# Optimization experiments

Measured on AMD Instinct MI355X. Metric: run time of the kernel, lower is better.

Reference implementation:

```python
import jax, jax.numpy as jnp
import numpy as np

B, T, D = 4, 256, 512          # batch, seq_len, encoder_dim
L, H = 2, 8                    # num xLSTM blocks, num heads
I = 2 * D                      # inner dim (proj_factor=2)
DH = I // H                    # per-head dim = 128
K, G = 32, 64                  # mdn_components, goal_dim
EPS = 1e-5


def _ln(x, s, b):
    m = x.mean(-1, keepdims=True)
    v = jnp.mean((x - m) ** 2, -1, keepdims=True)
    return (x - m) * jax.lax.rsqrt(v + EPS) * s + b


def setup_inputs() -> dict:
    key = jax.random.key(0)
    ks = jax.random.split(key, 16)
    sc = 0.02
    nrm = lambda k, shp: jax.random.normal(k, shp, jnp.float32) * sc
    return {
        "x": jax.random.normal(ks[0], (B, T, D), jnp.float32),
        "ln_s": jnp.ones((L, D), jnp.float32),
        "ln_b": jnp.zeros((L, D), jnp.float32),
        "W_proj": nrm(ks[1], (L, D, 2 * I)),
        "Wq": nrm(ks[2], (L, I, I)),
        "Wk": nrm(ks[3], (L, I, I)),
        "Wv": nrm(ks[4], (L, I, I)),
        "Wi": nrm(ks[5], (L, I, H)),
        "bi": jnp.zeros((L, H), jnp.float32),
        "Wf": nrm(ks[6], (L, I, H)),
        "bf": jnp.full((L, H), 3.0, jnp.float32),  # forget-gate bias init
        "gn_s": jnp.ones((L, I), jnp.float32),
        "gn_b": jnp.zeros((L, I), jnp.float32),
        "W_down": nrm(ks[7], (L, I, D)),
        "fln_s": jnp.ones((D,), jnp.float32),
        "fln_b": jnp.zeros((D,), jnp.float32),
        "W_pi": nrm(ks[8], (D, K)),
        "b_pi": jnp.zeros((K,), jnp.float32),
        "W_mu": nrm(ks[9], (D, K * G)),
        "b_mu": jnp.zeros((K * G,), jnp.float32),
        "W_sig": nrm(ks[10], (D, K * G)),
        "b_sig": jnp.zeros((K * G,), jnp.float32),
    }


def _forward(x, ln_s, ln_b, W_proj, Wq, Wk, Wv, Wi, bi, Wf, bf,
             gn_s, gn_b, W_down, fln_s, fln_b,
             W_pi, b_pi, W_mu, b_mu, W_sig, b_sig):
    inv_sqrt_dh = 1.0 / (DH ** 0.5)

    def step(carry, x_t):  # x_t: (B, D); replicates per-timestep xlstm_stack.step()
        C, n, m = carry    # (L,B,H,DH,DH), (L,B,H,DH), (L,B,H)
        h = x_t
        for l in range(L):  # fixed small block loop
            skip = h
            xn = _ln(h, ln_s[l], ln_b[l])
            xp = xn @ W_proj[l]                      # (B, 2I)
            xm, z = jnp.split(xp, 2, axis=-1)        # mLSTM branch / gate branch
            q = (xm @ Wq[l]).reshape(B, H, DH)
            k = (xm @ Wk[l]).reshape(B, H, DH) * inv_sqrt_dh
            v = (xm @ Wv[l]).reshape(B, H, DH)
            ip = xm @ Wi[l] + bi[l]                  # (B, H) exp input gate preact
            fp = xm @ Wf[l] + bf[l]                  # (B, H) forget gate preact
            logf = jax.nn.log_sigmoid(fp)
            m_new = jnp.maximum(logf + m[l], ip)     # stabilizer
            ig = jnp.exp(ip - m_new)
            fg = jnp.exp(logf + m[l] - m_new)
            # matrix memory update: C <- f*C + i * k v^T ; n <- f*n + i*k
            C_new = fg[:, :, None, None] * C[l] + ig[:, :, None, None] * (k[..., :, None] * v[..., None, :])
            n_new = fg[..., None] * n[l] + ig[..., None] * k
            num = jnp.einsum('bhk,bhkv->bhv', q, C_new)
            den = jnp.maximum(jnp.abs(jnp.einsum('bhk,bhk->bh', q, n_new)), 1.0)
            hh = num / den[..., None]                # (B, H, DH)
            # multi-head norm (per-head layernorm, no per-head affine)
            mu_h = hh.mean(-1, keepdims=True)
            var_h = jnp.mean((hh - mu_h) ** 2, -1, keepdims=True)
            hh = (hh - mu_h) * jax.lax.rsqrt(var_h + EPS)
            hh = hh.reshape(B, I) * gn_s[l] + gn_b[l]
            hh = hh * jax.nn.silu(z)                 # output gating branch
            h = skip + hh @ W_down[l]                # residual
            C = C.at[l].set(C_new)
            n = n.at[l].set(n_new)
            m = m.at[l].set(m_new)
        return (C, n, m), h

    C0 = jnp.zeros((L, B, H, DH, DH), x.dtype)
    n0 = jnp.zeros((L, B, H, DH), x.dtype)
    m0 = jnp.zeros((L, B, H), x.dtype)
    _, hs = jax.lax.scan(step, (C0, n0, m0), jnp.swapaxes(x, 0, 1))
    last = _ln(hs[-1], fln_s, fln_b)                 # post-blocks norm on final step
    pi = jax.nn.softmax(last @ W_pi + b_pi, axis=-1)              # (B, K)
    mu = (last @ W_mu + b_mu).reshape(B, K, G)                     # (B, K, G)
    sigma = jax.nn.softplus(last @ W_sig + b_sig).reshape(B, K, G) # (B, K, G)
    return pi, mu, sigma


def reference(x, ln_s, ln_b, W_proj, Wq, Wk, Wv, Wi, bi, Wf, bf,
              gn_s, gn_b, W_down, fln_s, fln_b,
              W_pi, b_pi, W_mu, b_mu, W_sig, b_sig):
    return _forward(x, ln_s, ln_b, W_proj, Wq, Wk, Wv, Wi, bi, Wf, bf,
                    gn_s, gn_b, W_down, fln_s, fln_b,
                    W_pi, b_pi, W_mu, b_mu, W_sig, b_sig)
```

## Files before the change

### kernel.cpp

```cpp
#include <hip/hip_runtime.h>
#include <hip/hip_bf16.h>
#include <math.h>

#define DEV __device__ __forceinline__

typedef __attribute__((ext_vector_type(8))) short bf16x8;
typedef __attribute__((ext_vector_type(4))) float f32x4;

static DEV float softplus_f(float x){ return fmaxf(x,0.f) + log1pf(expf(-fabsf(x))); }
static DEV float logsig_f(float x){ return fminf(x,0.f) - log1pf(expf(-fabsf(x))); }
static DEV float silu_f(float x){ return x / (1.f + expf(-x)); }
static DEV unsigned short f2bf(float f){
  union { float f; unsigned u; } v; v.f = f;
  unsigned r = (v.u + 0x7fffu + ((v.u >> 16) & 1u)) >> 16;
  return (unsigned short)r;
}
static DEV float bf2f(unsigned short u){
  union { unsigned u; float f; } v; v.u = ((unsigned)u) << 16; return v.f;
}
static DEV void load_lds16(const unsigned short* g, unsigned short* lds){
  __builtin_amdgcn_global_load_lds(
      (const __attribute__((address_space(1))) void*)g,
      (__attribute__((address_space(3))) void*)lds, 16, 0, 0);
}

__global__ __launch_bounds__(256) void wprep(
    const float* __restrict__ Wp, const float* __restrict__ Wq,
    const float* __restrict__ Wk, const float* __restrict__ Wv,
    const float* __restrict__ Wd, const float* __restrict__ Wi,
    const float* __restrict__ Wf,
    unsigned short* projT0, unsigned short* projT1,
    unsigned short* qT0, unsigned short* kT0, unsigned short* kT1,
    unsigned short* vT0, unsigned short* vT1, unsigned short* dT0,
    float* __restrict__ Wc)
{
  int bid = blockIdx.x;
  if (bid >= 1920){
    int fb = bid - 1920;
    int gid = fb * 4 + (threadIdx.x >> 6);
    int l = gid >> 9, d = gid & 511;
    int lane = threadIdx.x & 63;
    const float* wp = Wp + (size_t)l*512*2048 + (size_t)d*2048 + lane*16;
    const float* wi = Wi + (size_t)l*1024*8;
    const float* wf = Wf + (size_t)l*1024*8;
    float acc[16];
    #pragma unroll
    for (int q = 0; q < 16; ++q) acc[q] = 0.f;
    #pragma unroll 4
    for (int u = 0; u < 16; ++u){
      float xv = wp[u];
      int j = lane*16 + u;
      float4 wi0 = *(const float4*)(wi + j*8);
      float4 wi1 = *(const float4*)(wi + j*8 + 4);
      float4 wf0 = *(const float4*)(wf + j*8);
      float4 wf1 = *(const float4*)(wf + j*8 + 4);
      acc[0]  = fmaf(xv, wi0.x, acc[0]);  acc[1]  = fmaf(xv, wi0.y, acc[1]);
      acc[2]  = fmaf(xv, wi0.z, acc[2]);  acc[3]  = fmaf(xv, wi0.w, acc[3]);
      acc[4]  = fmaf(xv, wi1.x, acc[4]);  acc[5]  = fmaf(xv, wi1.y, acc[5]);
      acc[6]  = fmaf(xv, wi1.z, acc[6]);  acc[7]  = fmaf(xv, wi1.w, acc[7]);
      acc[8]  = fmaf(xv, wf0.x, acc[8]);  acc[9]  = fmaf(xv, wf0.y, acc[9]);
      acc[10] = fmaf(xv, wf0.z, acc[10]); acc[11] = fmaf(xv, wf0.w, acc[11]);
      acc[12] = fmaf(xv, wf1.x, acc[12]); acc[13] = fmaf(xv, wf1.y, acc[13]);
      acc[14] = fmaf(xv, wf1.z, acc[14]); acc[15] = fmaf(xv, wf1.w, acc[15]);
    }
    #pragma unroll
    for (int o = 32; o > 0; o >>= 1){
      #pragma unroll
      for (int q = 0; q < 16; ++q) acc[q] += __shfl_xor(acc[q], o);
    }
    if (lane == 0){
      float* dst = Wc + (size_t)l*512*16 + d*16;
      #pragma unroll
      for (int q = 0; q < 16; ++q) dst[q] = acc[q];
    }
    return;
  }
  int z, t;
  if (bid < 512){ z = bid >> 8; t = bid & 255; }
  else if (bid < 1792){ z = 2 + ((bid - 512) >> 8); t = (bid - 512) & 255; }
  else { z = 7; t = bid - 1792; }
  const float* W; unsigned short* Wt; int K, M; float scale = 1.f;
  const float INV = 0.08838834764831845f;
  switch (z){
    case 0: W = Wp;              Wt = projT0; K = 512;  M = 2048; break;
    case 1: W = Wp + 512*2048;   Wt = projT1; K = 512;  M = 2048; break;
    case 2: W = Wq;              Wt = qT0;    K = 1024; M = 1024; break;
    case 3: W = Wk;              Wt = kT0;    K = 1024; M = 1024; scale = INV; break;
    case 4: W = Wk + 1048576;    Wt = kT1;    K = 1024; M = 1024; scale = INV; break;
    case 5: W = Wv;              Wt = vT0;    K = 1024; M = 1024; break;
    case 6: W = Wv + 1048576;    Wt = vT1;    K = 1024; M = 1024; break;
    default: W = Wd;             Wt = dT0;    K = 1024; M = 512;  break;
  }
  int mtiles = M >> 6;
  int mt = t % mtiles, kt = t / mtiles;
  int m0 = mt * 64, k0 = kt * 64;
  __shared__ float s[64][65];
  int tx = threadIdx.x & 15, ty = threadIdx.x >> 4;
  #pragma unroll
  for (int u = 0; u < 64; u += 16){
    int r = u + ty;
    *(float4*)&s[r][tx*4] = *(const float4*)(W + (size_t)(k0+r)*M + m0 + tx*4);
  }
  __syncthreads();
  #pragma unroll
  for (int u = 0; u < 64; u += 16){
    int mr = u + ty;
    ushort4 o;
    o.x = f2bf(s[tx*4+0][mr] * scale);
    o.y = f2bf(s[tx*4+1][mr] * scale);
    o.z = f2bf(s[tx*4+2][mr] * scale);
    o.w = f2bf(s[tx*4+3][mr] * scale);
    *(ushort4*)(Wt + (size_t)(m0+mr)*K + k0 + tx*4) = o;
  }
}

__global__ __launch_bounds__(256) void ln_gates(
    const float* __restrict__ in, unsigned short* __restrict__ outb,
    const float* __restrict__ s, const float* __restrict__ b,
    const float* __restrict__ Wc, float* __restrict__ ipfp)
{
  int r = blockIdx.x;
  const float* x = in + (size_t)r * 512;
  int tid = threadIdx.x;
  float lsum = 0.f, lsq = 0.f;
  for (int i = tid; i < 512; i += 256){ float v = x[i]; lsum += v; lsq += v*v; }
  #pragma unroll
  for (int o = 32; o > 0; o >>= 1){ lsum += __shfl_down(lsum, o); lsq += __shfl_down(lsq, o); }
  __shared__ float s1[4], s2[4];
  int wid = tid >> 6, lane = tid & 63;
  if (lane == 0){ s1[wid] = lsum; s2[wid] = lsq; }
  __syncthreads();
  if (tid == 0){ float a=0.f,c=0.f; for (int w=0; w<4; ++w){ a+=s1[w]; c+=s2[w]; } s1[0]=a; s2[0]=c; }
  __syncthreads();
  float mean = s1[0] * (1.f/512.f);
  float var  = s2[0] * (1.f/512.f) - mean*mean;
  float rstd = rsqrtf(var + 1e-5f);
  __shared__ float P[256][17];
  float g[16];
  #pragma unroll
  for (int q = 0; q < 16; ++q) g[q] = 0.f;
  for (int i = tid; i < 512; i += 256){
    float v = (x[i]-mean)*rstd*s[i] + b[i];
    outb[(size_t)r*512 + i] = f2bf(v);
    const float* wrow = Wc + i*16;
    #pragma unroll
    for (int q = 0; q < 16; ++q) g[q] = fmaf(v, wrow[q], g[q]);
  }
  #pragma unroll
  for (int q = 0; q < 16; ++q) P[tid][q] = g[q];
  __syncthreads();
  {
    int q = tid >> 4, c = tid & 15;
    float sacc = 0.f;
    #pragma unroll
    for (int u = 0; u < 16; ++u) sacc += P[c*16 + u][q];
    sacc += __shfl_xor(sacc, 1); sacc += __shfl_xor(sacc, 2);
    sacc += __shfl_xor(sacc, 4); sacc += __shfl_xor(sacc, 8);
    if (c == 0) ipfp[r*16 + q] = sacc;
  }
}

__global__ __launch_bounds__(256) void gemm_mfma128_multi(
    const unsigned short* __restrict__ A, int lda,
    const unsigned short* __restrict__ Bt0, const unsigned short* __restrict__ Bt1,
    const unsigned short* __restrict__ Bt2, int ldb,
    unsigned short* __restrict__ C0, unsigned short* __restrict__ C1,
    unsigned short* __restrict__ C2, int ldc, int K)
{
  const unsigned short* Bt = (blockIdx.z == 0) ? Bt0 : (blockIdx.z == 1) ? Bt1 : Bt2;
  unsigned short* Cbf      = (blockIdx.z == 0) ? C0  : (blockIdx.z == 1) ? C1  : C2;
  __shared__ __align__(16) unsigned short As[8192];
  __shared__ __align__(16) unsigned short Bs[8192];
  int row0 = blockIdx.y * 128, col0 = blockIdx.x * 128;
  int tid = threadIdx.x;
  int w = tid >> 6, l = tid & 63;
  int wr = (w >> 1) * 64, wc = (w & 1) * 64;
  int lrm = l & 15, lk = l >> 4;
  int lr3 = l >> 3;
  int scc = (l & 7) ^ lr3;
  f32x4 acc[4][4] = {};
  for (int k0 = 0; k0 < K; k0 += 64){
    #pragma unroll
    for (int it = 0; it < 4; ++it){
      int rowA = (it*4 + w)*8 + lr3;
      load_lds16(A  + (size_t)(row0 + rowA)*lda + k0 + scc*8, &As[(it*4 + w)*512]);
      load_lds16(Bt + (size_t)(col0 + rowA)*ldb + k0 + scc*8, &Bs[(it*4 + w)*512]);
    }
    __syncthreads();
    #pragma unroll
    for (int kk = 0; kk < 2; ++kk){
      int q = kk*4 + lk;
      bf16x8 af[4], bfr[4];
      #pragma unroll
      for (int i = 0; i < 4; ++i){
        int ra = wr + i*16 + lrm;
        af[i] = *(const bf16x8*)&As[ra*64 + ((q ^ (ra & 7)) << 3)];
      }
      #pragma unroll
      for (int j = 0; j < 4; ++j){
        int rb = wc + j*16 + lrm;
        bfr[j] = *(const bf16x8*)&Bs[rb*64 + ((q ^ (rb & 7)) << 3)];
      }
      #pragma unroll
      for (int i = 0; i < 4; ++i)
        #pragma unroll
        for (int j = 0; j < 4; ++j)
          acc[i][j] = __builtin_amdgcn_mfma_f32_16x16x32_bf16(af[i], bfr[j], acc[i][j], 0, 0, 0);
    }
    __syncthreads();
  }
  #pragma unroll
  for (int i = 0; i < 4; ++i){
    #pragma unroll
    for (int j = 0; j < 4; ++j){
      int col = col0 + wc + j*16 + lrm;
      #pragma unroll
      for (int r = 0; r < 4; ++r){
        int row = row0 + wr + i*16 + lk*4 + r;
        Cbf[(size_t)row*ldc + col] = f2bf(acc[i][j][r]);
      }
    }
  }
}

__global__ __launch_bounds__(256) void gemm_mfma(
    const unsigned short* __restrict__ A, int lda,
    const unsigned short* __restrict__ Bt, int ldb,
    float* __restrict__ C, int ldc,
    unsigned short* __restrict__ Cbf,
    const float* __restrict__ skip, int ldskip,
    int K)
{
  __shared__ __align__(16) unsigned short As[64][72];
  __shared__ __align__(16) unsigned short Bs[64][72];
  int row0 = blockIdx.y * 64, col0 = blockIdx.x * 64;
  int tid = threadIdx.x;
  int w = tid >> 6, l = tid & 63;
  int wr = (w >> 1) * 32, wc = (w & 1) * 32;
  int lr = l & 15, lk = l >> 4;
  int r1 = tid >> 3, c1 = (tid & 7) * 8;
  int r2 = (tid + 256) >> 3, c2 = ((tid + 256) & 7) * 8;
  const unsigned short* a1 = A  + (size_t)(row0 + r1) * lda + c1;
  const unsigned short* a2 = A  + (size_t)(row0 + r2) * lda + c2;
  const unsigned short* b1 = Bt + (size_t)(col0 + r1) * ldb + c1;
  const unsigned short* b2 = Bt + (size_t)(col0 + r2) * ldb + c2;
  f32x4 acc00 = {0,0,0,0}, acc01 = {0,0,0,0}, acc10 = {0,0,0,0}, acc11 = {0,0,0,0};
  for (int k0 = 0; k0 < K; k0 += 64){
    *(bf16x8*)&As[r1][c1] = *(const bf16x8*)(a1 + k0);
    *(bf16x8*)&As[r2][c2] = *(const bf16x8*)(a2 + k0);
    *(bf16x8*)&Bs[r1][c1] = *(const bf16x8*)(b1 + k0);
    *(bf16x8*)&Bs[r2][c2] = *(const bf16x8*)(b2 + k0);
    __syncthreads();
    #pragma unroll
    for (int kk = 0; kk < 2; ++kk){
      bf16x8 a0 = *(const bf16x8*)&As[wr + lr][kk*32 + lk*8];
      bf16x8 a1f = *(const bf16x8*)&As[wr + 16 + lr][kk*32 + lk*8];
      bf16x8 b0 = *(const bf16x8*)&Bs[wc + lr][kk*32 + lk*8];
      bf16x8 b1f = *(const bf16x8*)&Bs[wc + 16 + lr][kk*32 + lk*8];
      acc00 = __builtin_amdgcn_mfma_f32_16x16x32_bf16(a0, b0, acc00, 0, 0, 0);
      acc01 = __builtin_amdgcn_mfma_f32_16x16x32_bf16(a0, b1f, acc01, 0, 0, 0);
      acc10 = __builtin_amdgcn_mfma_f32_16x16x32_bf16(a1f, b0, acc10, 0, 0, 0);
      acc11 = __builtin_amdgcn_mfma_f32_16x16x32_bf16(a1f, b1f, acc11, 0, 0, 0);
    }
    __syncthreads();
  }
  #pragma unroll
  for (int i = 0; i < 2; ++i){
    #pragma unroll
    for (int j = 0; j < 2; ++j){
      f32x4 a = (i == 0) ? ((j == 0) ? acc00 : acc01) : ((j == 0) ? acc10 : acc11);
      int col = col0 + wc + j*16 + lr;
      #pragma unroll
      for (int r = 0; r < 4; ++r){
        int row = row0 + wr + i*16 + lk*4 + r;
        float o = a[r];
        if (skip) o += skip[(size_t)row*ldskip + col];
        if (C)   C[(size_t)row*ldc + col] = o;
        if (Cbf) Cbf[(size_t)row*ldc + col] = f2bf(o);
      }
    }
  }
}

__global__ __launch_bounds__(256) void attn_l0_mfma(
    const unsigned short* __restrict__ q, const unsigned short* __restrict__ k,
    const unsigned short* __restrict__ v,
    const float* __restrict__ ipfp, const float* __restrict__ bi, const float* __restrict__ bfg,
    const unsigned short* __restrict__ xpb,
    const float* __restrict__ gn_s, const float* __restrict__ gn_b,
    unsigned short* __restrict__ gated)
{
  __shared__ __align__(16) char smem[48128];
  unsigned short (*Ks)[136] = (unsigned short(*)[136])smem;
  unsigned short (*Vt)[72]  = (unsigned short(*)[72])(smem + 17408);
  unsigned short (*Ps)[72]  = (unsigned short(*)[72])(smem + 35840);
  float* invden = (float*)(smem + 45056);
  float (*denL)[64] = (float(*)[64])(smem + 45568);
  float* alpha_full = (float*)(smem + 46080);
  float* Mt_full    = (float*)(smem + 47104);
  float (*numf)[140] = (float(*)[140])smem;

  int blk = blockIdx.x;
  int tt = blk & 3, h = (blk >> 2) & 7, b = blk >> 5;
  int t0 = tt * 64;
  int tid = threadIdx.x;
  int w = tid >> 6, l = tid & 63;
  int wr = (w >> 1) * 32;
  int wc = (w & 1) * 32;
  int wd = (w & 1) * 64;
  int lrm = l & 15, lk = l >> 4;
  size_t headoff = (size_t)h * 128;

  {
    #pragma unroll
    for (int u = 0; u < 4; ++u){
      int o = u*256 + tid, row = o >> 4, oct = o & 15;
      *(bf16x8*)&Ks[row][oct*8] =
        *(const bf16x8*)(q + (size_t)(b*256 + t0 + row)*1024 + headoff + oct*8);
    }
    if (tid < 64){
      int lane = tid;
      float bih = bi[h], bfh = bfg[h];
      float lf[4], ip4[4];
      #pragma unroll
      for (int u = 0; u < 4; ++u){
        int r = b*256 + lane*4 + u;
        ip4[u] = ipfp[r*16 + h] + bih;
        lf[u]  = logsig_f(ipfp[r*16 + 8 + h] + bfh);
      }
      float c0 = lf[0], c1 = c0+lf[1], c2 = c1+lf[2], c3 = c2+lf[3];
      float tot = c3, pre = tot;
      #pragma unroll
      for (int o = 1; o < 64; o <<= 1){ float vv = __shfl_up(pre, o); if (lane >= o) pre += vv; }
      float excl = pre - tot;
      float al[4] = { ip4[0]-(excl+c0), ip4[1]-(excl+c1), ip4[2]-(excl+c2), ip4[3]-(excl+c3) };
      float lm[4];
      lm[0]=al[0]; lm[1]=fmaxf(lm[0],al[1]); lm[2]=fmaxf(lm[1],al[2]); lm[3]=fmaxf(lm[2],al[3]);
      float pm = lm[3];
      #pragma unroll
      for (int o = 1; o < 64; o <<= 1){ float vv = __shfl_up(pm, o); if (lane >= o) pm = fmaxf(pm, vv); }
      float pmexcl = __shfl_up(pm, 1);
      if (lane == 0) pmexcl = -3.4e38f;
      #pragma unroll
      for (int u = 0; u < 4; ++u){
        alpha_full[lane*4+u] = al[u];
        Mt_full[lane*4+u] = fmaxf(0.f, fmaxf(pmexcl, lm[u]));
      }
    }
    if (tid < 128) ((float*)denL)[tid] = 0.f;
  }
  __syncthreads();
  bf16x8 aq[2][4];
  #pragma unroll
  for (int i = 0; i < 2; ++i)
    #pragma unroll
    for (int kk = 0; kk < 4; ++kk)
      aq[i][kk] = *(const bf16x8*)&Ks[wr + i*16 + lrm][kk*32 + lk*8];
  __syncthreads();

  f32x4 pacc[2][4] = {};
  int ntile = tt + 1;

  for (int it = 0; it < ntile; ++it){
    int s0 = it * 64;
    #pragma unroll
    for (int u = 0; u < 4; ++u){
      int o = u*256 + tid, row = o >> 4, oct = o & 15;
      *(bf16x8*)&Ks[row][oct*8] =
        *(const bf16x8*)(k + (size_t)(b*256 + s0 + row)*1024 + headoff + oct*8);
    }
    #pragma unroll
    for (int u = 0; u < 2; ++u){
      int task = u*256 + tid;
      int sp = task & 31, oct = task >> 5;
      const unsigned short* vp = v + (size_t)(b*256 + s0 + sp*2)*1024 + headoff + oct*8;
      bf16x8 r0 = *(const bf16x8*)vp;
      bf16x8 r1 = *(const bf16x8*)(vp + 1024);
      #pragma unroll
      for (int j = 0; j < 8; ++j){
        unsigned lo = (unsigned short)r0[j];
        unsigned hi = (unsigned short)r1[j];
        *(unsigned*)&Vt[oct*8 + j][sp*2] = lo | (hi << 16);
      }
    }
    __syncthreads();

    f32x4 sacc[2][2] = {};
    #pragma unroll
    for (int kk = 0; kk < 4; ++kk){
      bf16x8 b0 = *(const bf16x8*)&Ks[wc + lrm][kk*32 + lk*8];
      bf16x8 b1 = *(const bf16x8*)&Ks[wc + 16 + lrm][kk*32 + lk*8];
      sacc[0][0] = __builtin_amdgcn_mfma_f32_16x16x32_bf16(aq[0][kk], b0, sacc[0][0], 0, 0, 0);
      sacc[0][1] = __builtin_amdgcn_mfma_f32_16x16x32_bf16(aq[0][kk], b1, sacc[0][1], 0, 0, 0);
      sacc[1][0] = __builtin_amdgcn_mfma_f32_16x16x32_bf16(aq[1][kk], b0, sacc[1][0], 0, 0, 0);
      sacc[1][1] = __builtin_amdgcn_mfma_f32_16x16x32_bf16(aq[1][kk], b1, sacc[1][1], 0, 0, 0);
    }

    bool diag = (it == ntile - 1);
    float av0 = alpha_full[s0 + wc + lrm];
    float av1 = alpha_full[s0 + wc + 16 + lrm];
    #pragma unroll
    for (int i = 0; i < 2; ++i){
      #pragma unroll
      for (int r = 0; r < 4; ++r){
        int tl = wr + i*16 + lk*4 + r;
        float mt = Mt_full[t0 + tl];
        float p0 = __expf(av0 - mt) * sacc[i][0][r];
        float p1 = __expf(av1 - mt) * sacc[i][1][r];
        if (diag){
          if (wc + lrm      > tl) p0 = 0.f;
          if (wc + 16 + lrm > tl) p1 = 0.f;
        }
        Ps[tl][wc + lrm]      = f2bf(p0);
        Ps[tl][wc + 16 + lrm] = f2bf(p1);
        float dv = p0 + p1;
        dv += __shfl_xor(dv, 1); dv += __shfl_xor(dv, 2);
        dv += __shfl_xor(dv, 4); dv += __shfl_xor(dv, 8);
        if (lrm == 0) denL[w & 1][tl] += dv;
      }
    }
    __syncthreads();

    #pragma unroll
    for (int ks = 0; ks < 2; ++ks){
      bf16x8 pa0 = *(const bf16x8*)&Ps[wr + lrm][ks*32 + lk*8];
      bf16x8 pa1 = *(const bf16x8*)&Ps[wr + 16 + lrm][ks*32 + lk*8];
      #pragma unroll
      for (int jd = 0; jd < 4; ++jd){
        bf16x8 vb8 = *(const bf16x8*)&Vt[wd + jd*16 + lrm][ks*32 + lk*8];
        pacc[0][jd] = __builtin_amdgcn_mfma_f32_16x16x32_bf16(pa0, vb8, pacc[0][jd], 0, 0, 0);
        pacc[1][jd] = __builtin_amdgcn_mfma_f32_16x16x32_bf16(pa1, vb8, pacc[1][jd], 0, 0, 0);
      }
    }
    __syncthreads();
  }

  #pragma unroll
  for (int i = 0; i < 2; ++i)
    #pragma unroll
    for (int jd = 0; jd < 4; ++jd)
      #pragma unroll
      for (int r = 0; r < 4; ++r)
        numf[wr + i*16 + lk*4 + r][wd + jd*16 + lrm] = pacc[i][jd][r];
  if (tid < 64){
    float s = denL[0][tid] + denL[1][tid];
    invden[tid] = 1.0f / fmaxf(fabsf(s), 1.0f);
  }
  __syncthreads();

  {
    int row = tid >> 2, qq = tid & 3;
    float inv = invden[row];
    const float* nr = &numf[row][qq*32];
    float xs[32];
    float sum = 0.f, sq = 0.f;
    #pragma unroll
    for (int j = 0; j < 8; ++j){
      float4 t4 = *(const float4*)(nr + j*4);
      float v0 = t4.x*inv, v1 = t4.y*inv, v2 = t4.z*inv, v3 = t4.w*inv;
      xs[j*4+0] = v0; xs[j*4+1] = v1; xs[j*4+2] = v2; xs[j*4+3] = v3;
      sum += v0+v1+v2+v3;
      sq  += v0*v0+v1*v1+v2*v2+v3*v3;
    }
    sum += __shfl_xor(sum, 1); sq += __shfl_xor(sq, 1);
    sum += __shfl_xor(sum, 2); sq += __shfl_xor(sq, 2);
    float mean = sum * (1.f/128.f);
    float var  = sq  * (1.f/128.f) - mean*mean;
    float rstd = rsqrtf(var + 1e-5f);
    int rr = b*256 + t0 + row;
    const unsigned short* zp = xpb + (size_t)rr*2048 + 1024 + headoff + qq*32;
    const float* gsP = gn_s + headoff + qq*32;
    const float* gbP = gn_b + headoff + qq*32;
    unsigned short* op = gated + (size_t)rr*1024 + headoff + qq*32;
    #pragma unroll
    for (int j8 = 0; j8 < 4; ++j8){
      bf16x8 zv = *(const bf16x8*)(zp + j8*8);
      bf16x8 ov;
      #pragma unroll
      for (int j = 0; j < 8; ++j){
        int jj = j8*8 + j;
        float valn = (xs[jj]-mean)*rstd*gsP[jj] + gbP[jj];
        ov[j] = (short)f2bf(valn * silu_f(bf2f((unsigned short)zv[j])));
      }
      *(bf16x8*)(op + j8*8) = ov;
    }
  }
}

__global__ void qlast_split(const unsigned short* __restrict__ xpb, const float* __restrict__ Wq1,
                            float* __restrict__ part)
{
  int jt = blockIdx.x, ks = blockIdx.y;
  int j = jt*256 + threadIdx.x;
  __shared__ float xs[4][32];
  int t = threadIdx.x;
  if (t < 128){ int b = t >> 5, kk = t & 31; xs[b][kk] = bf2f(xpb[(size_t)(b*256+255)*2048 + ks*32 + kk]); }
  __syncthreads();
  float a0=0.f,a1=0.f,a2=0.f,a3=0.f;
  #pragma unroll 8
  for (int kk = 0; kk < 32; ++kk){
    float wv = Wq1[(size_t)(ks*32+kk)*1024 + j];
    a0 = fmaf(xs[0][kk], wv, a0);
    a1 = fmaf(xs[1][kk], wv, a1);
    a2 = fmaf(xs[2][kk], wv, a2);
    a3 = fmaf(xs[3][kk], wv, a3);
  }
  part[((size_t)ks*4 + 0)*1024 + j] = a0;
  part[((size_t)ks*4 + 1)*1024 + j] = a1;
  part[((size_t)ks*4 + 2)*1024 + j] = a2;
  part[((size_t)ks*4 + 3)*1024 + j] = a3;
}

__global__ __launch_bounds__(256) void attn_l1_split(
    const float* __restrict__ qpart, const unsigned short* __restrict__ k1,
    const unsigned short* __restrict__ v1,
    const float* __restrict__ ipfp, const float* __restrict__ bi, const float* __restrict__ bfg,
    float* __restrict__ pnum, float* __restrict__ pden)
{
  int sc = blockIdx.x, bh = blockIdx.y;
  int b = bh >> 3, h = bh & 7;
  int s0 = sc * 32;
  int tid = threadIdx.x;
  __shared__ float qsh[128];
  __shared__ float alpha256[256];
  __shared__ float mt255s;
  __shared__ float sred[32][9];
  __shared__ float as[32];
  __shared__ float nred[2][128];
  if (tid < 128){
    float s = 0.f;
    #pragma unroll 8
    for (int ks = 0; ks < 32; ++ks) s += qpart[((size_t)ks*4 + b)*1024 + h*128 + tid];
    qsh[tid] = s;
  }
  if (tid >= 128 && tid < 192){
    int lane = tid - 128;
    float bih = bi[h], bfh = bfg[h];
    float lf[4], ip4[4];
    #pragma unroll
    for (int u = 0; u < 4; ++u){
      int r = b*256 + lane*4 + u;
      ip4[u] = ipfp[r*16 + h] + bih;
      lf[u]  = logsig_f(ipfp[r*16 + 8 + h] + bfh);
    }
    float c0 = lf[0], c1 = c0+lf[1], c2 = c1+lf[2], c3 = c2+lf[3];
    float tot = c3, pre = tot;
    #pragma unroll
    for (int o = 1; o < 64; o <<= 1){ float vv = __shfl_up(pre, o); if (lane >= o) pre += vv; }
    float excl = pre - tot;
    float al[4] = { ip4[0]-(excl+c0), ip4[1]-(excl+c1), ip4[2]-(excl+c2), ip4[3]-(excl+c3) };
    #pragma unroll
    for (int u = 0; u < 4; ++u) alpha256[lane*4+u] = al[u];
    float mx = fmaxf(fmaxf(al[0],al[1]), fmaxf(al[2],al[3]));
    #pragma unroll
    for (int o = 32; o > 0; o >>= 1) mx = fmaxf(mx, __shfl_xor(mx, o));
    if (lane == 0) mt255s = fmaxf(0.f, mx);
  }
  __syncthreads();
  {
    int sl = tid & 31, dc = tid >> 5;
    const unsigned short* kp = k1 + (size_t)(b*256 + s0 + sl)*1024 + h*128 + dc*16;
    float p = 0.f;
    #pragma unroll
    for (int u = 0; u < 16; u += 8){
      bf16x8 kv = *(const bf16x8*)(kp + u);
      #pragma unroll
      for (int e = 0; e < 8; ++e) p = fmaf(qsh[dc*16+u+e], bf2f((unsigned short)kv[e]), p);
    }
    sred[sl][dc] = p;
  }
  __syncthreads();
  if (tid < 32){
    float sum = 0.f;
    #pragma unroll
    for (int dc = 0; dc < 8; ++dc) sum += sred[tid][dc];
    float w = __expf(alpha256[s0 + tid] - mt255s);
    as[tid] = w * sum;
  }
  __syncthreads();
  {
    int d = tid & 127, sg = tid >> 7;
    const unsigned short* vp = v1 + (size_t)(b*256 + s0 + sg*16)*1024 + h*128 + d;
    float np = 0.f;
    #pragma unroll
    for (int u = 0; u < 16; ++u) np = fmaf(as[sg*16 + u], bf2f(vp[(size_t)u*1024]), np);
    nred[sg][d] = np;
  }
  __syncthreads();
  if (tid < 128) pnum[((size_t)bh*8 + sc)*128 + tid] = nred[0][tid] + nred[1][tid];
  if (tid == 128){
    float dsum = 0.f;
    #pragma unroll
    for (int u = 0; u < 32; ++u) dsum += as[u];
    pden[bh*8 + sc] = dsum;
  }
}

__global__ __launch_bounds__(128) void attn_l1_fin(
    const float* __restrict__ pnum, const float* __restrict__ pden,
    const unsigned short* __restrict__ xpb,
    const float* __restrict__ gn_s, const float* __restrict__ gn_b,
    float* __restrict__ gated1)
{
  int bh = blockIdx.x; int b = bh >> 3, h = bh & 7;
  int tid = threadIdx.x;
  __shared__ float hh[128];
  __shared__ float dsh, msh, rsh;
  float nsum = 0.f;
  #pragma unroll
  for (int sc = 0; sc < 8; ++sc) nsum += pnum[((size_t)bh*8 + sc)*128 + tid];
  if (tid == 0){
    float d = 0.f;
    #pragma unroll
    for (int sc = 0; sc < 8; ++sc) d += pden[bh*8 + sc];
    dsh = fmaxf(fabsf(d), 1.0f);
  }
  __syncthreads();
  float hv = nsum / dsh;
  hh[tid] = hv;
  __syncthreads();
  if (tid < 64){
    float a = hh[tid], c = hh[tid + 64];
    float s1 = a + c, s2v = a*a + c*c;
    #pragma unroll
    for (int o = 32; o > 0; o >>= 1){ s1 += __shfl_down(s1, o); s2v += __shfl_down(s2v, o); }
    if (tid == 0){
      float mean = s1*(1.f/128.f);
      float var  = s2v*(1.f/128.f) - mean*mean;
      msh = mean; rsh = rsqrtf(var + 1e-5f);
    }
  }
  __syncthreads();
  {
    int i = h*128 + tid;
    float valn = (hv - msh)*rsh*gn_s[i] + gn_b[i];
    float z = bf2f(xpb[(size_t)(b*256 + 255)*2048 + 1024 + i]);
    gated1[b*1024 + i] = valn * silu_f(z);
  }
}

__global__ void dl_split(const float* __restrict__ gated1, const float* __restrict__ Wd,
                         float* __restrict__ part)
{
  int jt = blockIdx.x, ks = blockIdx.y;
  int j = jt*256 + threadIdx.x;
  __shared__ float xs[4][32];
  int t = threadIdx.x;
  if (t < 128){ int b = t >> 5, kk = t & 31; xs[b][kk] = gated1[b*1024 + ks*32 + kk]; }
  __syncthreads();
  float a0=0.f,a1=0.f,a2=0.f,a3=0.f;
  #pragma unroll 8
  for (int kk = 0; kk < 32; ++kk){
    float wv = Wd[(size_t)(ks*32+kk)*512 + j];
    a0 = fmaf(xs[0][kk], wv, a0);
    a1 = fmaf(xs[1][kk], wv, a1);
    a2 = fmaf(xs[2][kk], wv, a2);
    a3 = fmaf(xs[3][kk], wv, a3);
  }
  part[((size_t)ks*4 + 0)*512 + j] = a0;
  part[((size_t)ks*4 + 1)*512 + j] = a1;
  part[((size_t)ks*4 + 2)*512 + j] = a2;
  part[((size_t)ks*4 + 3)*512 + j] = a3;
}

__global__ __launch_bounds__(256) void dl_fin(
    const float* __restrict__ part, const float* __restrict__ h0,
    const float* __restrict__ fln_s, const float* __restrict__ fln_b,
    const float* __restrict__ W_pi, const float* __restrict__ b_pi,
    float* __restrict__ lastb, float* __restrict__ out)
{
  int b = blockIdx.x;
  int tid = threadIdx.x;
  __shared__ float ls[512];
  __shared__ float pred[8][33];
  __shared__ float s1[4], s2[4];
  float v[2];
  #pragma unroll
  for (int u = 0; u < 2; ++u){
    int jj = tid*2 + u;
    float s = 0.f;
    #pragma unroll 8
    for (int ks = 0; ks < 32; ++ks) s += part[((size_t)ks*4 + b)*512 + jj];
    v[u] = h0[(size_t)(b*256 + 255)*512 + jj] + s;
  }
  float lsum = v[0] + v[1], lsq = v[0]*v[0] + v[1]*v[1];
  #pragma unroll
  for (int o = 32; o > 0; o >>= 1){ lsum += __shfl_down(lsum, o); lsq += __shfl_down(lsq, o); }
  int wid = tid >> 6, lane = tid & 63;
  if (lane == 0){ s1[wid] = lsum; s2[wid] = lsq; }
  __syncthreads();
  if (tid == 0){ float a=0.f,c=0.f; for (int w2=0; w2<4; ++w2){ a+=s1[w2]; c+=s2[w2]; } s1[0]=a; s2[0]=c; }
  __syncthreads();
  float mean = s1[0] * (1.f/512.f);
  float var  = s2[0] * (1.f/512.f) - mean*mean;
  float rstd = rsqrtf(var + 1e-5f);
  #pragma unroll
  for (int u = 0; u < 2; ++u){
    int jj = tid*2 + u;
    float lv = (v[u]-mean)*rstd*fln_s[jj] + fln_b[jj];
    lastb[b*512 + jj] = lv;
    ls[jj] = lv;
  }
  __syncthreads();
  {
    int o = tid & 31, pt = tid >> 5;
    float pa = 0.f;
    #pragma unroll 8
    for (int u = 0; u < 64; ++u){ int i = pt*64 + u; pa = fmaf(ls[i], W_pi[i*32 + o], pa); }
    pred[pt][o] = pa;
  }
  __syncthreads();
  if (tid < 32){
    float acc = b_pi[tid];
    #pragma unroll
    for (int pt = 0; pt < 8; ++pt) acc += pred[pt][tid];
    float m = acc;
    #pragma unroll
    for (int o2 = 16; o2 > 0; o2 >>= 1) m = fmaxf(m, __shfl_xor(m, o2));
    float e = __expf(acc - m);
    float ss = e;
    #pragma unroll
    for (int o2 = 16; o2 > 0; o2 >>= 1) ss += __shfl_xor(ss, o2);
    out[b*32 + tid] = e / ss;
  }
}

__global__ void ms_split(const float* __restrict__ last,
                         const float* __restrict__ W_mu, const float* __restrict__ W_sig,
                         float* __restrict__ part)
{
  int jt = blockIdx.x, ks = blockIdx.y, mat = blockIdx.z;
  int j = jt*256 + threadIdx.x;
  const float* W = mat ? W_sig : W_mu;
  __shared__ float xs[4][64];
  int t = threadIdx.x;
  { int b = t >> 6, kk = t & 63; xs[b][kk] = last[b*512 + ks*64 + kk]; }
  __syncthreads();
  float a0=0.f,a1=0.f,a2=0.f,a3=0.f;
  #pragma unroll 8
  for (int kk = 0; kk < 64; ++kk){
    float wv = W[(size_t)(ks*64+kk)*2048 + j];
    a0 = fmaf(xs[0][kk], wv, a0);
    a1 = fmaf(xs[1][kk], wv, a1);
    a2 = fmaf(xs[2][kk], wv, a2);
    a3 = fmaf(xs[3][kk], wv, a3);
  }
  size_t base = ((size_t)(mat*8 + ks)*4);
  part[(base + 0)*2048 + j] = a0;
  part[(base + 1)*2048 + j] = a1;
  part[(base + 2)*2048 + j] = a2;
  part[(base + 3)*2048 + j] = a3;
}

__global__ void ms_reduce(const float* __restrict__ part,
                          const float* __restrict__ b_mu, const float* __restrict__ b_sig,
                          float* __restrict__ out)
{
  int j = blockIdx.x*256 + threadIdx.x;
  int b = blockIdx.y, mat = blockIdx.z;
  float s = mat ? b_sig[j] : b_mu[j];
  for (int ks = 0; ks < 8; ++ks) s += part[((size_t)(mat*8 + ks)*4 + b)*2048 + j];
  out[128 + mat*8192 + b*2048 + j] = mat ? softplus_f(s) : s;
}

extern "C" void kernel_launch(void* const* d_in, const int* in_sizes, int n_in,
                              void* d_out, int out_size, void* d_ws, size_t ws_size,
                              hipStream_t stream)
{
  const float* x      = (const float*)d_in[0];
  const float* ln_s   = (const float*)d_in[1];
  const float* ln_b   = (const float*)d_in[2];
  const float* W_proj = (const float*)d_in[3];
  const float* Wq     = (const float*)d_in[4];
  const float* Wk     = (const float*)d_in[5];
  const float* Wv     = (const float*)d_in[6];
  const float* Wi     = (const float*)d_in[7];
  const float* bi     = (const float*)d_in[8];
  const float* Wf     = (const float*)d_in[9];
  const float* bf     = (const float*)d_in[10];
  const float* gn_s   = (const float*)d_in[11];
  const float* gn_b   = (const float*)d_in[12];
  const float* W_down = (const float*)d_in[13];
  const float* fln_s  = (const float*)d_in[14];
  const float* fln_b  = (const float*)d_in[15];
  const float* W_pi   = (const float*)d_in[16];
  const float* b_pi   = (const float*)d_in[17];
  const float* W_mu   = (const float*)d_in[18];
  const float* b_mu   = (const float*)d_in[19];
  const float* W_sig  = (const float*)d_in[20];
  const float* b_sig  = (const float*)d_in[21];
  float* out = (float*)d_out;

  char* p = (char*)d_ws;
  unsigned short* projT0 = (unsigned short*)p; p += (size_t)2048*512*2;
  unsigned short* projT1 = (unsigned short*)p; p += (size_t)2048*512*2;
  unsigned short* qT0    = (unsigned short*)p; p += (size_t)1024*1024*2;
  unsigned short* kT0    = (unsigned short*)p; p += (size_t)1024*1024*2;
  unsigned short* kT1    = (unsigned short*)p; p += (size_t)1024*1024*2;
  unsigned short* vT0    = (unsigned short*)p; p += (size_t)1024*1024*2;
  unsigned short* vT1    = (unsigned short*)p; p += (size_t)1024*1024*2;
  unsigned short* dT0    = (unsigned short*)p; p += (size_t)512*1024*2;
  float* Wc              = (float*)p;          p += (size_t)2*512*16*4;
  unsigned short* xnb    = (unsigned short*)p; p += (size_t)1024*512*2;
  unsigned short* xpb    = (unsigned short*)p; p += (size_t)1024*2048*2;
  unsigned short* qbb    = (unsigned short*)p; p += (size_t)1024*1024*2;
  unsigned short* kbb    = (unsigned short*)p; p += (size_t)1024*1024*2;
  unsigned short* vbb    = (unsigned short*)p; p += (size_t)1024*1024*2;
  unsigned short* gatedb = (unsigned short*)p; p += (size_t)1024*1024*2;
  float* h0     = (float*)p; p += (size_t)1024*512*4;
  float* ipfp   = (float*)p; p += (size_t)16384*4;
  float* gated1 = (float*)p; p += (size_t)4096*4;
  float* lastb  = (float*)p; p += (size_t)2048*4;
  float* qpart  = (float*)p; p += (size_t)32*4096*4;
  float* dpart  = (float*)p; p += (size_t)32*4*512*4;
  float* pnum   = (float*)p; p += (size_t)32*8*128*4;
  float* pden   = (float*)p; p += (size_t)32*8*4;
  float* mspart = (float*)p; p += (size_t)16*4*2048*4;

  const float* ln_s1 = ln_s + 512;
  const float* ln_b1 = ln_b + 512;
  const float* gn_s1 = gn_s + 1024;
  const float* gn_b1 = gn_b + 1024;
  const float* Wq1   = Wq + 1024*1024;
  const float* Wd1   = W_down + 1024*512;

  dim3 blk256(256);

  wprep<<<2176, blk256, 0, stream>>>(W_proj, Wq, Wk, Wv, W_down, Wi, Wf,
      projT0, projT1, qT0, kT0, kT1, vT0, vT1, dT0, Wc);

  ln_gates<<<1024, blk256, 0, stream>>>(x, xnb, ln_s, ln_b, Wc, ipfp);
  gemm_mfma128_multi<<<dim3(16,8,1), blk256, 0, stream>>>(xnb, 512, projT0, projT0, projT0, 512, xpb, xpb, xpb, 2048, 512);
  gemm_mfma128_multi<<<dim3(8,8,3), blk256, 0, stream>>>(xpb, 2048, qT0, kT0, vT0, 1024, qbb, kbb, vbb, 1024, 1024);
  attn_l0_mfma<<<128, blk256, 0, stream>>>(qbb, kbb, vbb, ipfp, bi, bf, xpb, gn_s, gn_b, gatedb);
  gemm_mfma<<<dim3(8,16), blk256, 0, stream>>>(gatedb, 1024, dT0, 1024, h0, 512, nullptr, x, 512, 1024);

  ln_gates<<<1024, blk256, 0, stream>>>(h0, xnb, ln_s1, ln_b1, Wc + 512*16, ipfp);
  gemm_mfma128_multi<<<dim3(16,8,1), blk256, 0, stream>>>(xnb, 512, projT1, projT1, projT1, 512, xpb, xpb, xpb, 2048, 512);
  gemm_mfma128_multi<<<dim3(8,8,2), blk256, 0, stream>>>(xpb, 2048, kT1, vT1, vT1, 1024, kbb, vbb, vbb, 1024, 1024);
  qlast_split<<<dim3(4,32), blk256, 0, stream>>>(xpb, Wq1, qpart);
  attn_l1_split<<<dim3(8,32), blk256, 0, stream>>>(qpart, kbb, vbb, ipfp, bi + 8, bf + 8, pnum, pden);
  attn_l1_fin<<<32, 128, 0, stream>>>(pnum, pden, xpb, gn_s1, gn_b1, gated1);
  dl_split<<<dim3(2,32), blk256, 0, stream>>>(gated1, Wd1, dpart);
  dl_fin<<<4, blk256, 0, stream>>>(dpart, h0, fln_s, fln_b, W_pi, b_pi, lastb, out);

  ms_split<<<dim3(8,8,2), blk256, 0, stream>>>(lastb, W_mu, W_sig, mspart);
  ms_reduce<<<dim3(8,4,2), blk256, 0, stream>>>(mspart, b_mu, b_sig, out);
}
```

Before: 192.1 us.

## Fuse split-reduce kernel pairs with last-block atomic finalization; widen weight-transpose tiles

Merges three split/finalize kernel pairs (attention layer-1, down-projection plus final norm and pi softmax, mu/sigma heads) into single kernels. The last block to finish, found through an atomic counter after a threadfence, performs the reduction, which removes three kernel launches and their serialization gaps. Counters are zeroed in the weight-prep kernel. The weight-transpose blocks now cover 128-row K tiles with 8-wide bf16 stores, halving the block count. The costs are that each finalize step runs on one block, and that correctness depends on the counter reset and memory fences.

```diff
diff --git a/kernel.cpp b/kernel.cpp
--- a/kernel.cpp
+++ b/kernel.cpp
@@ -32,11 +32,12 @@
     unsigned short* projT0, unsigned short* projT1,
     unsigned short* qT0, unsigned short* kT0, unsigned short* kT1,
     unsigned short* vT0, unsigned short* vT1, unsigned short* dT0,
-    float* __restrict__ Wc)
+    float* __restrict__ Wc, unsigned* __restrict__ cnts)
 {
   int bid = blockIdx.x;
-  if (bid >= 1920){
-    int fb = bid - 1920;
+  if (bid == 0 && threadIdx.x < 40) cnts[threadIdx.x] = 0;
+  if (bid >= 960){
+    int fb = bid - 960;
     int gid = fb * 4 + (threadIdx.x >> 6);
     int l = gid >> 9, d = gid & 511;
     int lane = threadIdx.x & 63;
@@ -76,9 +77,8 @@
     return;
   }
   int z, t;
-  if (bid < 512){ z = bid >> 8; t = bid & 255; }
-  else if (bid < 1792){ z = 2 + ((bid - 512) >> 8); t = (bid - 512) & 255; }
-  else { z = 7; t = bid - 1792; }
+  if (bid < 896){ z = bid >> 7; t = bid & 127; }
+  else { z = 7; t = bid - 896; }
   const float* W; unsigned short* Wt; int K, M; float scale = 1.f;
   const float INV = 0.08838834764831845f;
   switch (z){
@@ -93,11 +93,11 @@
   }
   int mtiles = M >> 6;
   int mt = t % mtiles, kt = t / mtiles;
-  int m0 = mt * 64, k0 = kt * 64;
-  __shared__ float s[64][65];
+  int m0 = mt * 64, k0 = kt * 128;
+  __shared__ float s[128][65];
   int tx = threadIdx.x & 15, ty = threadIdx.x >> 4;
   #pragma unroll
-  for (int u = 0; u < 64; u += 16){
+  for (int u = 0; u < 128; u += 16){
     int r = u + ty;
     *(float4*)&s[r][tx*4] = *(const float4*)(W + (size_t)(k0+r)*M + m0 + tx*4);
   }
@@ -105,12 +105,10 @@
   #pragma unroll
   for (int u = 0; u < 64; u += 16){
     int mr = u + ty;
-    ushort4 o;
-    o.x = f2bf(s[tx*4+0][mr] * scale);
-    o.y = f2bf(s[tx*4+1][mr] * scale);
-    o.z = f2bf(s[tx*4+2][mr] * scale);
-    o.w = f2bf(s[tx*4+3][mr] * scale);
-    *(ushort4*)(Wt + (size_t)(m0+mr)*K + k0 + tx*4) = o;
+    bf16x8 o;
+    #pragma unroll
+    for (int e = 0; e < 8; ++e) o[e] = (short)f2bf(s[tx*8+e][mr] * scale);
+    *(bf16x8*)(Wt + (size_t)(m0+mr)*K + k0 + tx*8) = o;
   }
 }
 
@@ -515,7 +513,10 @@
     const float* __restrict__ qpart, const unsigned short* __restrict__ k1,
     const unsigned short* __restrict__ v1,
     const float* __restrict__ ipfp, const float* __restrict__ bi, const float* __restrict__ bfg,
-    float* __restrict__ pnum, float* __restrict__ pden)
+    const unsigned short* __restrict__ xpb,
+    const float* __restrict__ gn_s, const float* __restrict__ gn_b,
+    float* __restrict__ pnum, float* __restrict__ pden,
+    float* __restrict__ gated1, unsigned* __restrict__ cnts)
 {
   int sc = blockIdx.x, bh = blockIdx.y;
   int b = bh >> 3, h = bh & 7;
@@ -594,59 +595,60 @@
     for (int u = 0; u < 32; ++u) dsum += as[u];
     pden[bh*8 + sc] = dsum;
   }
-}
-
-__global__ __launch_bounds__(128) void attn_l1_fin(
-    const float* __restrict__ pnum, const float* __restrict__ pden,
-    const unsigned short* __restrict__ xpb,
-    const float* __restrict__ gn_s, const float* __restrict__ gn_b,
-    float* __restrict__ gated1)
-{
-  int bh = blockIdx.x; int b = bh >> 3, h = bh & 7;
-  int tid = threadIdx.x;
-  __shared__ float hh[128];
-  __shared__ float dsh, msh, rsh;
-  float nsum = 0.f;
-  #pragma unroll
-  for (int sc = 0; sc < 8; ++sc) nsum += pnum[((size_t)bh*8 + sc)*128 + tid];
+  __threadfence();
+  __shared__ int lastF;
+  if (tid == 0) lastF = (atomicAdd(&cnts[2 + bh], 1u) == 7u) ? 1 : 0;
+  __syncthreads();
+  if (!lastF) return;
+  __shared__ float hh2[128];
+  __shared__ float dsh2, msh2, rsh2;
   if (tid == 0){
     float d = 0.f;
     #pragma unroll
-    for (int sc = 0; sc < 8; ++sc) d += pden[bh*8 + sc];
-    dsh = fmaxf(fabsf(d), 1.0f);
-  }
-  __syncthreads();
-  float hv = nsum / dsh;
-  hh[tid] = hv;
+    for (int s2 = 0; s2 < 8; ++s2) d += pden[bh*8 + s2];
+    dsh2 = fmaxf(fabsf(d), 1.0f);
+  }
+  __syncthreads();
+  if (tid < 128){
+    float nsum = 0.f;
+    #pragma unroll
+    for (int s2 = 0; s2 < 8; ++s2) nsum += pnum[((size_t)bh*8 + s2)*128 + tid];
+    hh2[tid] = nsum / dsh2;
+  }
   __syncthreads();
   if (tid < 64){
-    float a = hh[tid], c = hh[tid + 64];
+    float a = hh2[tid], c = hh2[tid + 64];
     float s1 = a + c, s2v = a*a + c*c;
     #pragma unroll
     for (int o = 32; o > 0; o >>= 1){ s1 += __shfl_down(s1, o); s2v += __shfl_down(s2v, o); }
     if (tid == 0){
       float mean = s1*(1.f/128.f);
       float var  = s2v*(1.f/128.f) - mean*mean;
-      msh = mean; rsh = rsqrtf(var + 1e-5f);
-    }
-  }
-  __syncthreads();
-  {
+      msh2 = mean; rsh2 = rsqrtf(var + 1e-5f);
+    }
+  }
+  __syncthreads();
+  if (tid < 128){
     int i = h*128 + tid;
-    float valn = (hv - msh)*rsh*gn_s[i] + gn_b[i];
+    float valn = (hh2[tid] - msh2)*rsh2*gn_s[i] + gn_b[i];
     float z = bf2f(xpb[(size_t)(b*256 + 255)*2048 + 1024 + i]);
     gated1[b*1024 + i] = valn * silu_f(z);
   }
 }
 
-__global__ void dl_split(const float* __restrict__ gated1, const float* __restrict__ Wd,
-                         float* __restrict__ part)
+__global__ __launch_bounds__(256) void dl_all(
+    const float* __restrict__ gated1, const float* __restrict__ Wd,
+    const float* __restrict__ h0,
+    const float* __restrict__ fln_s, const float* __restrict__ fln_b,
+    const float* __restrict__ W_pi, const float* __restrict__ b_pi,
+    float* __restrict__ part, float* __restrict__ lastb, float* __restrict__ out,
+    unsigned* __restrict__ cnts)
 {
   int jt = blockIdx.x, ks = blockIdx.y;
   int j = jt*256 + threadIdx.x;
+  int tid = threadIdx.x;
   __shared__ float xs[4][32];
-  int t = threadIdx.x;
-  if (t < 128){ int b = t >> 5, kk = t & 31; xs[b][kk] = gated1[b*1024 + ks*32 + kk]; }
+  if (tid < 128){ int b = tid >> 5, kk = tid & 31; xs[b][kk] = gated1[b*1024 + ks*32 + kk]; }
   __syncthreads();
   float a0=0.f,a1=0.f,a2=0.f,a3=0.f;
   #pragma unroll 8
@@ -661,80 +663,81 @@
   part[((size_t)ks*4 + 1)*512 + j] = a1;
   part[((size_t)ks*4 + 2)*512 + j] = a2;
   part[((size_t)ks*4 + 3)*512 + j] = a3;
-}
-
-__global__ __launch_bounds__(256) void dl_fin(
-    const float* __restrict__ part, const float* __restrict__ h0,
-    const float* __restrict__ fln_s, const float* __restrict__ fln_b,
-    const float* __restrict__ W_pi, const float* __restrict__ b_pi,
-    float* __restrict__ lastb, float* __restrict__ out)
-{
-  int b = blockIdx.x;
+  __threadfence();
+  __shared__ int lastF;
+  if (tid == 0) lastF = (atomicAdd(&cnts[0], 1u) == 63u) ? 1 : 0;
+  __syncthreads();
+  if (!lastF) return;
+  __shared__ float ls2[512];
+  __shared__ float pred2[8][33];
+  __shared__ float s1[4], s2[4];
+  for (int b2 = 0; b2 < 4; ++b2){
+    float v[2];
+    #pragma unroll
+    for (int u = 0; u < 2; ++u){
+      int jj = tid*2 + u;
+      float s = 0.f;
+      #pragma unroll 8
+      for (int k2 = 0; k2 < 32; ++k2) s += part[((size_t)k2*4 + b2)*512 + jj];
+      v[u] = h0[(size_t)(b2*256 + 255)*512 + jj] + s;
+    }
+    float lsum = v[0] + v[1], lsq = v[0]*v[0] + v[1]*v[1];
+    #pragma unroll
+    for (int o = 32; o > 0; o >>= 1){ lsum += __shfl_down(lsum, o); lsq += __shfl_down(lsq, o); }
+    int wid = tid >> 6, lane = tid & 63;
+    if (lane == 0){ s1[wid] = lsum; s2[wid] = lsq; }
+    __syncthreads();
+    if (tid == 0){ float a=0.f,c=0.f; for (int w2=0; w2<4; ++w2){ a+=s1[w2]; c+=s2[w2]; } s1[0]=a; s2[0]=c; }
+    __syncthreads();
+    float mean = s1[0] * (1.f/512.f);
+    float var  = s2[0] * (1.f/512.f) - mean*mean;
+    float rstd = rsqrtf(var + 1e-5f);
+    #pragma unroll
+    for (int u = 0; u < 2; ++u){
+      int jj = tid*2 + u;
+      float lv = (v[u]-mean)*rstd*fln_s[jj] + fln_b[jj];
+      lastb[b2*512 + jj] = lv;
+      ls2[jj] = lv;
+    }
+    __syncthreads();
+    {
+      int o = tid & 31, pt = tid >> 5;
+      float pa = 0.f;
+      #pragma unroll 8
+      for (int u = 0; u < 64; ++u){ int i = pt*64 + u; pa = fmaf(ls2[i], W_pi[i*32 + o], pa); }
+      pred2[pt][o] = pa;
+    }
+    __syncthreads();
+    if (tid < 32){
+      float acc = b_pi[tid];
+      #pragma unroll
+      for (int pt = 0; pt < 8; ++pt) acc += pred2[pt][tid];
+      float m = acc;
+      #pragma unroll
+      for (int o2 = 16; o2 > 0; o2 >>= 1) m = fmaxf(m, __shfl_xor(m, o2));
+      float e = __expf(acc - m);
+      float ss = e;
+      #pragma unroll
+      for (int o2 = 16; o2 > 0; o2 >>= 1) ss += __shfl_xor(ss, o2);
+      out[b2*32 + tid] = e / ss;
+    }
+    __syncthreads();
+  }
+}
+
+__global__ __launch_bounds__(256) void ms_all(
+    const float* __restrict__ last,
+    const float* __restrict__ W_mu, const float* __restrict__ W_sig,
+    const float* __restrict__ b_mu, const float* __restrict__ b_sig,
+    float* __restrict__ part, float* __restrict__ out,
+    unsigned* __restrict__ cnts)
+{
+  int jt = blockIdx.x, ks = blockIdx.y, mat = blockIdx.z;
   int tid = threadIdx.x;
-  __shared__ float ls[512];
-  __shared__ float pred[8][33];
-  __shared__ float s1[4], s2[4];
-  float v[2];
-  #pragma unroll
-  for (int u = 0; u < 2; ++u){
-    int jj = tid*2 + u;
-    float s = 0.f;
-    #pragma unroll 8
-    for (int ks = 0; ks < 32; ++ks) s += part[((size_t)ks*4 + b)*512 + jj];
-    v[u] = h0[(size_t)(b*256 + 255)*512 + jj] + s;
-  }
-  float lsum = v[0] + v[1], lsq = v[0]*v[0] + v[1]*v[1];
-  #pragma unroll
-  for (int o = 32; o > 0; o >>= 1){ lsum += __shfl_down(lsum, o); lsq += __shfl_down(lsq, o); }
-  int wid = tid >> 6, lane = tid & 63;
-  if (lane == 0){ s1[wid] = lsum; s2[wid] = lsq; }
-  __syncthreads();
-  if (tid == 0){ float a=0.f,c=0.f; for (int w2=0; w2<4; ++w2){ a+=s1[w2]; c+=s2[w2]; } s1[0]=a; s2[0]=c; }
-  __syncthreads();
-  float mean = s1[0] * (1.f/512.f);
-  float var  = s2[0] * (1.f/512.f) - mean*mean;
-  float rstd = rsqrtf(var + 1e-5f);
-  #pragma unroll
-  for (int u = 0; u < 2; ++u){
-    int jj = tid*2 + u;
-    float lv = (v[u]-mean)*rstd*fln_s[jj] + fln_b[jj];
-    lastb[b*512 + jj] = lv;
-    ls[jj] = lv;
-  }
-  __syncthreads();
-  {
-    int o = tid & 31, pt = tid >> 5;
-    float pa = 0.f;
-    #pragma unroll 8
-    for (int u = 0; u < 64; ++u){ int i = pt*64 + u; pa = fmaf(ls[i], W_pi[i*32 + o], pa); }
-    pred[pt][o] = pa;
-  }
-  __syncthreads();
-  if (tid < 32){
-    float acc = b_pi[tid];
-    #pragma unroll
-    for (int pt = 0; pt < 8; ++pt) acc += pred[pt][tid];
-    float m = acc;
-    #pragma unroll
-    for (int o2 = 16; o2 > 0; o2 >>= 1) m = fmaxf(m, __shfl_xor(m, o2));
-    float e = __expf(acc - m);
-    float ss = e;
-    #pragma unroll
-    for (int o2 = 16; o2 > 0; o2 >>= 1) ss += __shfl_xor(ss, o2);
-    out[b*32 + tid] = e / ss;
-  }
-}
-
-__global__ void ms_split(const float* __restrict__ last,
-                         const float* __restrict__ W_mu, const float* __restrict__ W_sig,
-                         float* __restrict__ part)
-{
-  int jt = blockIdx.x, ks = blockIdx.y, mat = blockIdx.z;
-  int j = jt*256 + threadIdx.x;
+  int j = jt*256 + tid;
   const float* W = mat ? W_sig : W_mu;
   __shared__ float xs[4][64];
-  int t = threadIdx.x;
-  { int b = t >> 6, kk = t & 63; xs[b][kk] = last[b*512 + ks*64 + kk]; }
+  { int b = tid >> 6, kk = tid & 63; xs[b][kk] = last[b*512 + ks*64 + kk]; }
   __syncthreads();
   float a0=0.f,a1=0.f,a2=0.f,a3=0.f;
   #pragma unroll 8
@@ -750,17 +753,25 @@
   part[(base + 1)*2048 + j] = a1;
   part[(base + 2)*2048 + j] = a2;
   part[(base + 3)*2048 + j] = a3;
-}
-
-__global__ void ms_reduce(const float* __restrict__ part,
-                          const float* __restrict__ b_mu, const float* __restrict__ b_sig,
-                          float* __restrict__ out)
-{
-  int j = blockIdx.x*256 + threadIdx.x;
-  int b = blockIdx.y, mat = blockIdx.z;
-  float s = mat ? b_sig[j] : b_mu[j];
-  for (int ks = 0; ks < 8; ++ks) s += part[((size_t)(mat*8 + ks)*4 + b)*2048 + j];
-  out[128 + mat*8192 + b*2048 + j] = mat ? softplus_f(s) : s;
+  __threadfence();
+  __shared__ int lastF;
+  if (tid == 0) lastF = (atomicAdd(&cnts[1], 1u) == 127u) ? 1 : 0;
+  __syncthreads();
+  if (!lastF) return;
+  for (int it2 = 0; it2 < 8; ++it2){
+    int jj = it2*256 + tid;
+    #pragma unroll
+    for (int m2 = 0; m2 < 2; ++m2){
+      float bias = (m2 ? b_sig : b_mu)[jj];
+      #pragma unroll
+      for (int b2 = 0; b2 < 4; ++b2){
+        float s = bias;
+        #pragma unroll
+        for (int k2 = 0; k2 < 8; ++k2) s += part[((size_t)(m2*8 + k2)*4 + b2)*2048 + jj];
+        out[128 + m2*8192 + b2*2048 + jj] = m2 ? softplus_f(s) : s;
+      }
+    }
+  }
 }
 
 extern "C" void kernel_launch(void* const* d_in, const int* in_sizes, int n_in,
@@ -816,6 +827,7 @@
   float* pnum   = (float*)p; p += (size_t)32*8*128*4;
   float* pden   = (float*)p; p += (size_t)32*8*4;
   float* mspart = (float*)p; p += (size_t)16*4*2048*4;
+  unsigned* cnts = (unsigned*)p; p += 64*4;
 
   const float* ln_s1 = ln_s + 512;
   const float* ln_b1 = ln_b + 512;
@@ -826,8 +838,8 @@
 
   dim3 blk256(256);
 
-  wprep<<<2176, blk256, 0, stream>>>(W_proj, Wq, Wk, Wv, W_down, Wi, Wf,
-      projT0, projT1, qT0, kT0, kT1, vT0, vT1, dT0, Wc);
+  wprep<<<1216, blk256, 0, stream>>>(W_proj, Wq, Wk, Wv, W_down, Wi, Wf,
+      projT0, projT1, qT0, kT0, kT1, vT0, vT1, dT0, Wc, cnts);
 
   ln_gates<<<1024, blk256, 0, stream>>>(x, xnb, ln_s, ln_b, Wc, ipfp);
   gemm_mfma128_multi<<<dim3(16,8,1), blk256, 0, stream>>>(xnb, 512, projT0, projT0, projT0, 512, xpb, xpb, xpb, 2048, 512);
@@ -839,11 +851,10 @@
   gemm_mfma128_multi<<<dim3(16,8,1), blk256, 0, stream>>>(xnb, 512, projT1, projT1, projT1, 512, xpb, xpb, xpb, 2048, 512);
   gemm_mfma128_multi<<<dim3(8,8,2), blk256, 0, stream>>>(xpb, 2048, kT1, vT1, vT1, 1024, kbb, vbb, vbb, 1024, 1024);
   qlast_split<<<dim3(4,32), blk256, 0, stream>>>(xpb, Wq1, qpart);
-  attn_l1_split<<<dim3(8,32), blk256, 0, stream>>>(qpart, kbb, vbb, ipfp, bi + 8, bf + 8, pnum, pden);
-  attn_l1_fin<<<32, 128, 0, stream>>>(pnum, pden, xpb, gn_s1, gn_b1, gated1);
-  dl_split<<<dim3(2,32), blk256, 0, stream>>>(gated1, Wd1, dpart);
-  dl_fin<<<4, blk256, 0, stream>>>(dpart, h0, fln_s, fln_b, W_pi, b_pi, lastb, out);
-
-  ms_split<<<dim3(8,8,2), blk256, 0, stream>>>(lastb, W_mu, W_sig, mspart);
-  ms_reduce<<<dim3(8,4,2), blk256, 0, stream>>>(mspart, b_mu, b_sig, out);
-}
+  attn_l1_split<<<dim3(8,32), blk256, 0, stream>>>(qpart, kbb, vbb, ipfp, bi + 8, bf + 8,
+      xpb, gn_s1, gn_b1, pnum, pden, gated1, cnts);
+  dl_all<<<dim3(2,32), blk256, 0, stream>>>(gated1, Wd1, h0, fln_s, fln_b, W_pi, b_pi,
+      dpart, lastb, out, cnts);
+
+  ms_all<<<dim3(8,8,2), blk256, 0, stream>>>(lastb, W_mu, W_sig, b_mu, b_sig, mspart, out, cnts);
+}
```

Result: slower. 354.4 us (+84.5%).
